# Kernel tuning notes

Hardware: AMD Instinct MI355X
Metric: run time of the kernel (lower is better)

## Reference

```python
import jax, jax.numpy as jnp
import numpy as np

EPS_BN = 1e-5
EPS_NORM = 1e-12


def _conv1x1(x, W, b):
    # x: (B,C,H,W), W: (O,C), b: (O,)
    return jnp.einsum('bchw,oc->bohw', x, W) + b[None, :, None, None]


def _bn_train(x, gamma, beta):
    # BatchNorm2d in training mode: biased batch statistics over (N,H,W)
    m = x.mean(axis=(0, 2, 3), keepdims=True)
    v = x.var(axis=(0, 2, 3), keepdims=True)
    return (x - m) / jnp.sqrt(v + EPS_BN) * gamma[None, :, None, None] + beta[None, :, None, None]


def _l2norm(x):
    # F.normalize(dim=-1)
    return x / jnp.maximum(jnp.linalg.norm(x, axis=-1, keepdims=True), EPS_NORM)


def setup_inputs() -> dict:
    key = jax.random.key(0)
    ks = jax.random.split(key, 12)
    B, C, H, Wd = 8, 256, 64, 64
    HD, M = 128, 10
    s = 0.02
    inp = {
        'key': jax.random.normal(ks[0], (B, C, H, Wd), jnp.float32),
        'query': jax.random.normal(ks[1], (B, C, H, Wd), jnp.float32),
        'W_theta': jax.random.normal(ks[2], (HD, C), jnp.float32) * s,
        'b_theta': jnp.zeros((HD,), jnp.float32),
        'W_phi': jax.random.normal(ks[3], (HD, C), jnp.float32) * s,
        'b_phi': jnp.zeros((HD,), jnp.float32),
        'W_g': jax.random.normal(ks[4], (HD, C), jnp.float32) * s,
        'b_g': jnp.zeros((HD,), jnp.float32),
        'W_pc': jax.random.normal(ks[5], (HD, C), jnp.float32) * s,
        'b_pc': jnp.zeros((HD,), jnp.float32),
        'gamma_pc': jnp.ones((HD,), jnp.float32),
        'beta_pc': jnp.zeros((HD,), jnp.float32),
        'W_heads': jax.random.normal(ks[6], (M, HD), jnp.float32) * s,
        'W_o': jax.random.normal(ks[7], (C, HD), jnp.float32) * s,
        'b_o': jnp.zeros((C,), jnp.float32),
        'gamma_o': jnp.ones((C,), jnp.float32),
        'beta_o': jnp.zeros((C,), jnp.float32),
    }
    return inp


def reference(key, query, W_theta, b_theta, W_phi, b_phi, W_g, b_g,
              W_pc, b_pc, gamma_pc, beta_pc, W_heads, W_o, b_o, gamma_o, beta_o):
    B, C, H, Wd = key.shape
    HD = W_theta.shape[0]
    HW = H * Wd

    # --- non-local self-attention branch ---
    theta = _conv1x1(key, W_theta, b_theta).reshape(B, HD, HW)
    phi = _conv1x1(key, W_phi, b_phi).reshape(B, HD, HW)
    g = _conv1x1(key, W_g, b_g).reshape(B, HD, HW)
    att = jax.nn.softmax(jnp.einsum('bdn,bdm->bnm', theta, phi), axis=-1)  # (B,HW,HW)
    nlsa_out = jnp.einsum('bnm,bdm->bdn', att, g).reshape(B, HD, H, Wd)

    # --- prototype features ---
    key_f = jax.nn.relu(_bn_train(_conv1x1(key, W_pc, b_pc), gamma_pc, beta_pc))
    key_f = key_f.transpose(0, 2, 3, 1).reshape(B, HW, HD)  # (B,n,d); query_ == key_f

    mhw = jax.nn.softmax(key_f @ W_heads.T, axis=1)          # softmax over spatial dim
    protos = jnp.einsum('bnm,bnd->bmd', mhw, key_f)          # (B,M,d)

    # --- losses (training path) ---
    pn = _l2norm(protos)
    M = pn.shape[1]
    dis = 1.0 - ((pn[:, None, :, :] - pn[:, :, None, :]) ** 2)[None]  # (1,B,M,M,d)
    dis = dis * (dis > 0).astype(dis.dtype)
    dis = jnp.triu(dis, k=1)  # triu over last two dims (M,d), as torch.triu does
    dis_loss = (dis.sum(axis=1).sum(axis=1) * 2.0 / (M * (M - 1))).mean()
    cst_loss = ((pn[1:] - pn[:-1]) ** 2).sum(-1).mean()

    score = jnp.einsum('bnd,bmd->bnm', key_f, pn)            # (B,n,M)
    sp = jax.nn.softmax(score, axis=-1)                      # softmax over protos
    new_q = _l2norm(jnp.einsum('bnm,bmd->bnd', sp, pn))      # (B,n,d)

    idx = jnp.argmax(sp, axis=-1)                            # top-1 proto per position
    pos = pn[jnp.arange(B)[:, None], idx]                    # (B,n,d)
    fea_loss = jnp.mean((key_f - pos) ** 2)

    # --- output projection ---
    uq = new_q.transpose(0, 2, 1).reshape(B, HD, H, Wd) + nlsa_out
    out = jax.nn.relu(_bn_train(_conv1x1(uq, W_o, b_o), gamma_o, beta_o)) + query
    return out, fea_loss, cst_loss, dis_loss
```

## Files before the change

kernel.cpp:

```cpp
#include <hip/hip_runtime.h>
#include <stdint.h>

#define BB 8
#define CC 256
#define HDIM 128
#define NHW 4096
#define MM 10
#define OUTN (BB*CC*NHW)

typedef uint32_t u32;
typedef unsigned short u16;
using f32x4 = __attribute__((ext_vector_type(4))) float;
using bfv8  = __attribute__((ext_vector_type(8))) short;

__device__ __forceinline__ u16 f2bf(float f){
  union { float f; u32 u; } v; v.f = f;
  u32 u = v.u;
  u32 r = (u + 0x7fffu + ((u >> 16) & 1u)) >> 16;
  return (u16)r;
}

__device__ __forceinline__ float bf2f(u16 h){
  union { u32 u; float f; } v; v.u = ((u32)h) << 16; return v.f;
}

__device__ __forceinline__ f32x4 mfma16(bfv8 a, bfv8 b, f32x4 c){
  return __builtin_amdgcn_mfma_f32_16x16x32_bf16(a, b, c, 0, 0, 0);
}

__device__ __forceinline__ void gload16(const void* g, void* l){
  __builtin_amdgcn_global_load_lds((const __attribute__((address_space(1))) unsigned int*)g,
                                   (__attribute__((address_space(3))) unsigned int*)l, 16, 0, 0);
}

__global__ __launch_bounds__(256) void k0_keyt(const float* __restrict__ key, u16* __restrict__ keyT){
  __shared__ u16 sm[64][73];
  int blk = blockIdx.x;
  int b = blk & 7; int r = blk >> 3; int ct = r & 3; int nt = r >> 2;
  int n0 = nt*64, c0 = ct*64;
  int t = threadIdx.x; int nl = t & 63; int cl0 = t >> 6;
#pragma unroll
  for (int i = 0; i < 16; ++i){
    int cl = i*4 + cl0;
    sm[cl][nl] = f2bf(key[(size_t)(b*CC + c0 + cl)*NHW + n0 + nl]);
  }
  __syncthreads();
#pragma unroll
  for (int i = 0; i < 2; ++i){
    int j = i*256 + t; int nl2 = j >> 3; int c8 = j & 7;
    __align__(16) u16 tmp[8];
#pragma unroll
    for (int k = 0; k < 8; ++k) tmp[k] = sm[c8*8 + k][nl2];
    *(uint4*)&keyT[(size_t)(b*NHW + n0 + nl2)*CC + c0 + c8*8] = *(uint4*)tmp;
  }
}

__global__ __launch_bounds__(256) void k0b_w(const float* __restrict__ Wth, const float* __restrict__ Wph,
                                             const float* __restrict__ Wg, const float* __restrict__ Wpc,
                                             const float* __restrict__ Wo,
                                             u16* __restrict__ Wbf, u16* __restrict__ Wobf,
                                             float* __restrict__ stats, float* __restrict__ protos){
  int flat = blockIdx.x*256 + threadIdx.x;
  if (flat < 1540) stats[flat] = 0.f;
  if (flat < BB*MM*HDIM) protos[flat] = 0.f;
  int base = flat*4;
  u16 o4[4]; uint2 pk;
  if (base < 512*256){
    int o = base >> 8, c = base & 255;
    const float* srcs[4] = {Wth, Wph, Wg, Wpc};
    const float* sp = srcs[o >> 7] + (size_t)(o & 127)*256 + c;
#pragma unroll
    for (int j=0;j<4;++j) o4[j] = f2bf(sp[j]);
    pk.x = (u32)o4[0] | ((u32)o4[1]<<16); pk.y = (u32)o4[2] | ((u32)o4[3]<<16);
    *(uint2*)&Wbf[base] = pk;
  } else {
    int b2 = base - 512*256;
    const float* sp = Wo + b2;
#pragma unroll
    for (int j=0;j<4;++j) o4[j] = f2bf(sp[j]);
    pk.x = (u32)o4[0] | ((u32)o4[1]<<16); pk.y = (u32)o4[2] | ((u32)o4[3]<<16);
    *(uint2*)&Wobf[b2] = pk;
  }
}

__global__ __launch_bounds__(256) void k1_conv4(const u16* __restrict__ keyT, const u16* __restrict__ Wbf,
    const float* __restrict__ bth, const float* __restrict__ bph, const float* __restrict__ bg, const float* __restrict__ bpc,
    u16* __restrict__ thetaT, u16* __restrict__ phiT, u16* __restrict__ gN, float* __restrict__ pcraw)
{
  __shared__ __align__(16) u16 lds[64*256];
  int blk = blockIdx.x;
  int b = blk & 7; int nt = blk >> 3; int n0 = nt*64;
  int t = threadIdx.x; int w = t >> 6; int l = t & 63;
  int l15 = l & 15, l4 = l >> 4;
  const u16* src = keyT + (size_t)(b*NHW + n0)*CC;
#pragma unroll
  for (int i = 0; i < 8; ++i){
    int c = w*8 + i;
    int row = c*2 + (l >> 5);
    int wl = (l & 31) ^ (row & 7);
    gload16(src + (size_t)row*256 + wl*8, &lds[c*512]);
  }
  __syncthreads();
  int wn = w & 1, wo = w >> 1;
  bfv8 a[2][8];
#pragma unroll
  for (int nb = 0; nb < 2; ++nb)
#pragma unroll
    for (int kb = 0; kb < 8; ++kb){
      int row = wn*32 + nb*16 + l15;
      int wd = (kb*4 + l4) ^ (row & 7);
      a[nb][kb] = *(const bfv8*)&lds[row*256 + wd*8];
    }
  const float* bias[4] = {bth, bph, bg, bpc};
  const u16* wpbase = Wbf + (size_t)(wo*16*16 + l15)*256 + l4*8;
  bfv8 wc[8], wnx[8];
#pragma unroll
  for (int kb = 0; kb < 8; ++kb) wc[kb] = *(const bfv8*)&wpbase[kb*32];
  for (int ob = 0; ob < 16; ++ob){
    if (ob < 15){
      const u16* wp = wpbase + (size_t)(ob+1)*16*256;
#pragma unroll
      for (int kb = 0; kb < 8; ++kb) wnx[kb] = *(const bfv8*)&wp[kb*32];
    }
    f32x4 acc[2] = {{0,0,0,0},{0,0,0,0}};
#pragma unroll
    for (int kb = 0; kb < 8; ++kb){
      acc[0] = mfma16(a[0][kb], wc[kb], acc[0]);
      acc[1] = mfma16(a[1][kb], wc[kb], acc[1]);
    }
    int obg = wo*16 + ob;
    int seg = obg >> 3;
    int oo = (obg & 7)*16 + l15;
    float bv = bias[seg][oo];
#pragma unroll
    for (int nb = 0; nb < 2; ++nb)
#pragma unroll
      for (int rr = 0; rr < 4; ++rr){
        int n = n0 + wn*32 + nb*16 + l4*4 + rr;
        float v = acc[nb][rr] + bv;
        size_t off = ((size_t)(b*NHW + n))*HDIM + oo;
        if      (seg == 0) thetaT[off] = f2bf(v);
        else if (seg == 1) phiT[off]   = f2bf(v);
        else if (seg == 2) gN[off]     = f2bf(v);
        else               pcraw[off]  = v;
      }
#pragma unroll
    for (int kb = 0; kb < 8; ++kb) wc[kb] = wnx[kb];
  }
}

__global__ __launch_bounds__(256) void k1b_gt(const u16* __restrict__ gN, u16* __restrict__ gT){
  __shared__ __align__(16) u16 lds[64][72];
  int blk = blockIdx.x;
  int b = blk & 7; int r = blk >> 3; int nt = r & 63; int dt = r >> 6;
  int n0 = nt*64, d0 = dt*64;
  int t = threadIdx.x;
#pragma unroll
  for (int i = 0; i < 2; ++i){
    int seg = i*256 + t; int row = seg >> 3; int sg = seg & 7;
    *(uint4*)&lds[row][sg*8] = *(const uint4*)&gN[(size_t)(b*NHW + n0 + row)*HDIM + d0 + sg*8];
  }
  __syncthreads();
  int dr = t >> 2, ns = (t & 3)*16;
  __align__(16) u16 tmp[16];
#pragma unroll
  for (int j = 0; j < 16; ++j) tmp[j] = lds[ns + j][dr];
  u16* dst = gT + (size_t)(b*HDIM + d0 + dr)*NHW + n0 + ns;
  *(uint4*)&dst[0] = *(uint4*)&tmp[0];
  *(uint4*)&dst[8] = *(uint4*)&tmp[8];
}

__global__ __launch_bounds__(256) void k2_pcstats(const float* __restrict__ pcraw, float* __restrict__ stats){
  int blk = blockIdx.x;
  int b = blk >> 5; int ch = blk & 31; int n0 = ch*128;
  int t = threadIdx.x; int d = t & 127; int j = t >> 7;
  float s = 0, ss = 0;
  const float* p = pcraw + (size_t)(b*NHW + n0)*HDIM;
  for (int i = 0; i < 64; ++i){ float v = p[(size_t)(i*2 + j)*HDIM + d]; s += v; ss += v*v; }
  __shared__ float red[2][256];
  red[0][t] = s; red[1][t] = ss;
  __syncthreads();
  if (t < 128){
    atomicAdd(&stats[d],       red[0][t] + red[0][t+128]);
    atomicAdd(&stats[128 + d], red[1][t] + red[1][t+128]);
  }
}

__global__ __launch_bounds__(256) void k2b_keyf(const float* __restrict__ pcraw, const float* __restrict__ stats,
                                                const float* __restrict__ gamma, const float* __restrict__ beta,
                                                float* __restrict__ keyf){
  int idx = blockIdx.x*256 + threadIdx.x;
  int base = idx*4; int d0 = base & 127;
  f32x4 v = *(const f32x4*)&pcraw[base];
  f32x4 o;
#pragma unroll
  for (int j = 0; j < 4; ++j){
    int d = d0 + j;
    float mean = stats[d] * (1.f/32768.f);
    float var  = stats[128+d] * (1.f/32768.f) - mean*mean;
    if (var < 0.f) var = 0.f;
    float rstd = rsqrtf(var + 1e-5f);
    float x = (v[j] - mean) * rstd * gamma[d] + beta[d];
    o[j] = x > 0.f ? x : 0.f;
  }
  *(f32x4*)&keyf[base] = o;
}

__global__ __launch_bounds__(256) void k3_attn(const u16* __restrict__ thetaT, const u16* __restrict__ phiT,
                                               const u16* __restrict__ gT,
                                               u16* __restrict__ nl0, u16* __restrict__ nl1,
                                               u16* __restrict__ nl2, u16* __restrict__ nl3,
                                               float* __restrict__ lsumP){
  __shared__ __align__(16) u16 K2[2][32*128];
  __shared__ __align__(16) u16 V2[2][128*32];
  __shared__ __align__(16) u16 P[4][32*40];
  int blk = blockIdx.x;
  int b = blk & 7; int r1 = blk >> 3; int qt = r1 & 31; int split = r1 >> 5;
  int n0 = qt*128;
  int t = threadIdx.x; int w = t >> 6; int l = t & 63;
  int l15 = l & 15, l4 = l >> 4;
  bfv8 q[2][4];
#pragma unroll
  for (int nb = 0; nb < 2; ++nb){
    const u16* qp = thetaT + (size_t)(b*NHW + n0 + w*32 + nb*16 + l15)*HDIM + l4*8;
#pragma unroll
    for (int kb = 0; kb < 4; ++kb) q[nb][kb] = *(const bfv8*)&qp[kb*32];
  }
  float lsum[2][4];
  f32x4 acco[2][8];
#pragma unroll
  for (int nb=0; nb<2; ++nb){
#pragma unroll
    for (int rr=0; rr<4; ++rr) lsum[nb][rr] = 0.f;
#pragma unroll
    for (int db=0; db<8; ++db) acco[nb][db] = {0,0,0,0};
  }
  const u16* Kg = phiT + (size_t)b*NHW*HDIM;
  const u16* Vg = gT   + (size_t)b*HDIM*NHW;
  int mt0 = split*32;

#define STAGE(bf, mt) {                                                        \
    int m0 = (mt)*32;                                                          \
  _Pragma("unroll")                                                            \
    for (int i = 0; i < 2; ++i){                                               \
      int c = w*2 + i;                                                         \
      int row = c*4 + (l >> 4);                                                \
      int wl = (l & 15) ^ (row & 7);                                           \
      gload16(Kg + (size_t)(m0 + row)*HDIM + wl*8, &K2[bf][c*512]);            \
    }                                                                          \
  _Pragma("unroll")                                                            \
    for (int i = 0; i < 2; ++i){                                               \
      int c = w*2 + i;                                                         \
      int row = c*16 + (l >> 2);                                               \
      int wl = (l & 3) ^ (row & 3);                                            \
      gload16(Vg + (size_t)row*NHW + m0 + wl*8, &V2[bf][c*512]);               \
    }                                                                          \
  }

  STAGE(0, mt0);
  __syncthreads();
  int cur = 0;
  for (int it = 0; it < 32; ++it){
    if (it < 31) STAGE(cur^1, mt0 + it + 1);
    f32x4 s[2][2];
#pragma unroll
    for (int nb=0;nb<2;++nb){ s[nb][0] = {0,0,0,0}; s[nb][1] = {0,0,0,0}; }
    __builtin_amdgcn_s_setprio(1);
#pragma unroll
    for (int kb = 0; kb < 4; ++kb){
#pragma unroll
      for (int mb = 0; mb < 2; ++mb){
        int krow = mb*16 + l15;
        int kw = (kb*4 + l4) ^ (krow & 7);
        bfv8 kf = *(const bfv8*)&K2[cur][krow*128 + kw*8];
        s[0][mb] = mfma16(q[0][kb], kf, s[0][mb]);
        s[1][mb] = mfma16(q[1][kb], kf, s[1][mb]);
      }
    }
    __builtin_amdgcn_s_setprio(0);
#pragma unroll
    for (int nb = 0; nb < 2; ++nb)
#pragma unroll
      for (int mb = 0; mb < 2; ++mb)
#pragma unroll
        for (int rr = 0; rr < 4; ++rr){
          float p = __expf(s[nb][mb][rr]);
          lsum[nb][rr] += p;
          int prow = nb*16 + l4*4 + rr;
          int pcol = mb*16 + l15;
          P[w][prow*40 + pcol] = f2bf(p);
        }
    bfv8 pa[2];
#pragma unroll
    for (int nb=0;nb<2;++nb)
      pa[nb] = *(const bfv8*)&P[w][(nb*16 + l15)*40 + l4*8];
    __builtin_amdgcn_s_setprio(1);
#pragma unroll
    for (int db = 0; db < 8; ++db){
      int vrow = db*16 + l15;
      int vw = l4 ^ (vrow & 3);
      bfv8 vf = *(const bfv8*)&V2[cur][vrow*32 + vw*8];
      acco[0][db] = mfma16(pa[0], vf, acco[0][db]);
      acco[1][db] = mfma16(pa[1], vf, acco[1][db]);
    }
    __builtin_amdgcn_s_setprio(0);
    __syncthreads();
    cur ^= 1;
  }
#undef STAGE
  u16* nlsaP = (split==0) ? nl0 : (split==1) ? nl1 : (split==2) ? nl2 : nl3;
#pragma unroll
  for (int nb = 0; nb < 2; ++nb)
#pragma unroll
    for (int rr = 0; rr < 4; ++rr){
      float v = lsum[nb][rr];
      v += __shfl_xor(v, 1); v += __shfl_xor(v, 2); v += __shfl_xor(v, 4); v += __shfl_xor(v, 8);
      int n = n0 + w*32 + nb*16 + l4*4 + rr;
      if (l15 == 0) lsumP[(size_t)(split*8 + b)*NHW + n] = v;
      u16* op = nlsaP + ((size_t)(b*NHW + n))*HDIM;
#pragma unroll
      for (int db = 0; db < 8; ++db)
        op[db*16 + l15] = f2bf(acco[nb][db][rr]);
    }
}

__global__ __launch_bounds__(256) void k4_protos(const float* __restrict__ keyf, const float* __restrict__ Wh,
                                                 float* __restrict__ protos){
  __shared__ float wh[10][128];
  __shared__ float e[128][12];
  __shared__ float pacc[10][128];
  int blk = blockIdx.x; int b = blk & 7; int ns = blk >> 3;
  int n0 = ns*128;
  int t = threadIdx.x;
  for (int i = t; i < 1280; i += 256) wh[i>>7][i&127] = Wh[i];
  __syncthreads();
  const float* kf = keyf + ((size_t)b*NHW + n0)*HDIM;
  {
    int nn = t >> 1; int mh = (t & 1)*5;
    const f32x4* row = (const f32x4*)&kf[(size_t)nn*HDIM];
    float s5[5];
#pragma unroll
    for (int m = 0; m < 5; ++m) s5[m] = 0.f;
    for (int d4 = 0; d4 < 32; ++d4){
      f32x4 kv = row[d4];
#pragma unroll
      for (int m = 0; m < 5; ++m){
        f32x4 wv = *(const f32x4*)&wh[mh+m][d4*4];
        s5[m] += kv[0]*wv[0] + kv[1]*wv[1] + kv[2]*wv[2] + kv[3]*wv[3];
      }
    }
#pragma unroll
    for (int m = 0; m < 5; ++m) e[nn][mh+m] = __expf(s5[m]);
  }
  __syncthreads();
  int d = t & 127, j = t >> 7;
  float acc[10];
#pragma unroll
  for (int m = 0; m < 10; ++m) acc[m] = 0.f;
  for (int i = 0; i < 64; ++i){
    int n = j*64 + i;
    float kv = kf[(size_t)n*HDIM + d];
#pragma unroll
    for (int m = 0; m < 10; ++m) acc[m] += e[n][m]*kv;
  }
  if (j == 1){
#pragma unroll
    for (int m = 0; m < 10; ++m) pacc[m][d] = acc[m];
  }
  __syncthreads();
  if (j == 0){
#pragma unroll
    for (int m = 0; m < 10; ++m)
      atomicAdd(&protos[(size_t)(b*MM + m)*HDIM + d], acc[m] + pacc[m][d]);
  }
}

__global__ __launch_bounds__(64) void k5a_norm(float* __restrict__ protos){
  int row = blockIdx.x;
  int t = threadIdx.x;
  float v0 = protos[row*128 + t];
  float v1 = protos[row*128 + 64 + t];
  float ss = v0*v0 + v1*v1;
#pragma unroll
  for (int msk = 1; msk < 64; msk <<= 1) ss += __shfl_xor(ss, msk);
  float inv = 1.f / fmaxf(sqrtf(ss), 1e-12f);
  protos[row*128 + t]      = v0*inv;
  protos[row*128 + 64 + t] = v1*inv;
}

__global__ __launch_bounds__(128) void k5b_loss(const float* __restrict__ pn, float* __restrict__ stats){
  __shared__ float p0[10][128];
  __shared__ float p1[10][128];
  __shared__ float rd[2][2];
  int b = blockIdx.x;
  int t = threadIdx.x;
  for (int i = t; i < 1280; i += 128) p0[i>>7][i&127] = pn[(size_t)b*1280 + i];
  if (b < 7)
    for (int i = t; i < 1280; i += 128) p1[i>>7][i&127] = pn[(size_t)(b+1)*1280 + i];
  __syncthreads();
  int d = t;
  float dacc = 0.f;
#pragma unroll
  for (int m1 = 0; m1 < 10; ++m1){
    float a = p0[m1][d];
#pragma unroll
    for (int m2 = 0; m2 < 10; ++m2){
      if (d >= m2 + 1){
        float df = a - p0[m2][d];
        float v = 1.f - df*df;
        if (v > 0.f) dacc += v;
      }
    }
  }
  float cacc = 0.f;
  if (b < 7){
#pragma unroll
    for (int m = 0; m < 10; ++m){
      float df = p1[m][d] - p0[m][d];
      cacc += df*df;
    }
  }
#pragma unroll
  for (int msk = 1; msk < 64; msk <<= 1){ dacc += __shfl_xor(dacc, msk); cacc += __shfl_xor(cacc, msk); }
  int wv = t >> 6, ln = t & 63;
  if (ln == 0){ rd[0][wv] = dacc; rd[1][wv] = cacc; }
  __syncthreads();
  if (t == 0){
    atomicAdd(&stats[1537], rd[0][0] + rd[0][1]);
    atomicAdd(&stats[1538], rd[1][0] + rd[1][1]);
  }
}

__global__ __launch_bounds__(64) void k6_newq(const float* __restrict__ keyf, const float* __restrict__ pn,
                                              const u16* __restrict__ nl0, const u16* __restrict__ nl1,
                                              const u16* __restrict__ nl2, const u16* __restrict__ nl3,
                                              const float* __restrict__ lsumP,
                                              u16* __restrict__ uqbf, float* __restrict__ fea_acc){
  __shared__ float pnl[10][128];
  int blk = blockIdx.x;
  int b = blk & 7; int nt = blk >> 3;
  int t = threadIdx.x;
  for (int i = t; i < 1280; i += 64) pnl[i>>7][i&127] = pn[(size_t)b*1280 + i];
  __syncthreads();
  int n = nt*64 + t;
  const float* kf = keyf + (size_t)(b*NHW + n)*HDIM;
  float s[10];
#pragma unroll
  for (int m = 0; m < 10; ++m) s[m] = 0;
  for (int d4 = 0; d4 < 32; ++d4){
    f32x4 kv = *(const f32x4*)&kf[d4*4];
#pragma unroll
    for (int m = 0; m < 10; ++m){
      f32x4 pv = *(const f32x4*)&pnl[m][d4*4];
      s[m] += kv[0]*pv[0]+kv[1]*pv[1]+kv[2]*pv[2]+kv[3]*pv[3];
    }
  }
  float mx = s[0]; int idx = 0;
#pragma unroll
  for (int m = 1; m < 10; ++m) if (s[m] > mx){ mx = s[m]; idx = m; }
  float S_ = 0, sp[10];
#pragma unroll
  for (int m = 0; m < 10; ++m){ float ev = __expf(s[m]-mx); sp[m] = ev; S_ += ev; }
  float invS = 1.f/S_;
#pragma unroll
  for (int m = 0; m < 10; ++m) sp[m] *= invS;
  float ssq = 0, fea = 0;
  for (int d4 = 0; d4 < 32; ++d4){
    f32x4 kv = *(const f32x4*)&kf[d4*4];
    f32x4 a = {0,0,0,0};
#pragma unroll
    for (int m = 0; m < 10; ++m){
      f32x4 pv = *(const f32x4*)&pnl[m][d4*4];
      a[0] += sp[m]*pv[0]; a[1] += sp[m]*pv[1]; a[2] += sp[m]*pv[2]; a[3] += sp[m]*pv[3];
    }
    ssq += a[0]*a[0]+a[1]*a[1]+a[2]*a[2]+a[3]*a[3];
    f32x4 pb = *(const f32x4*)&pnl[idx][d4*4];
    float e0 = kv[0]-pb[0], e1 = kv[1]-pb[1], e2 = kv[2]-pb[2], e3 = kv[3]-pb[3];
    fea += e0*e0+e1*e1+e2*e2+e3*e3;
  }
  float inv = 1.f / fmaxf(sqrtf(ssq), 1e-12f);
  float ls = lsumP[(size_t)b*NHW + n] + lsumP[(size_t)(8+b)*NHW + n]
           + lsumP[(size_t)(16+b)*NHW + n] + lsumP[(size_t)(24+b)*NHW + n];
  float invl = 1.f/ls;
  const u16* na0 = nl0 + (size_t)(b*NHW + n)*HDIM;
  const u16* na1 = nl1 + (size_t)(b*NHW + n)*HDIM;
  const u16* na2 = nl2 + (size_t)(b*NHW + n)*HDIM;
  const u16* na3 = nl3 + (size_t)(b*NHW + n)*HDIM;
  u16* uo = uqbf + (size_t)(b*NHW + n)*HDIM;
  for (int d4 = 0; d4 < 32; ++d4){
    f32x4 a = {0,0,0,0};
#pragma unroll
    for (int m = 0; m < 10; ++m){
      f32x4 pv = *(const f32x4*)&pnl[m][d4*4];
      a[0] += sp[m]*pv[0]; a[1] += sp[m]*pv[1]; a[2] += sp[m]*pv[2]; a[3] += sp[m]*pv[3];
    }
    uint2 r0 = *(const uint2*)&na0[d4*4];
    uint2 r1 = *(const uint2*)&na1[d4*4];
    uint2 r2 = *(const uint2*)&na2[d4*4];
    uint2 r3 = *(const uint2*)&na3[d4*4];
    u16 o4[4];
#pragma unroll
    for (int j = 0; j < 4; ++j){
      u32 word0 = (j < 2) ? r0.x : r0.y;  u32 word1 = (j < 2) ? r1.x : r1.y;
      u32 word2 = (j < 2) ? r2.x : r2.y;  u32 word3 = (j < 2) ? r3.x : r3.y;
      int sh = (j & 1)*16;
      float nv = bf2f((u16)(word0 >> sh)) + bf2f((u16)(word1 >> sh))
               + bf2f((u16)(word2 >> sh)) + bf2f((u16)(word3 >> sh));
      o4[j] = f2bf(a[j]*inv + nv*invl);
    }
    uint2 pk; pk.x = (u32)o4[0] | ((u32)o4[1]<<16); pk.y = (u32)o4[2] | ((u32)o4[3]<<16);
    *(uint2*)&uo[d4*4] = pk;
  }
#pragma unroll
  for (int msk = 1; msk < 64; msk <<= 1) fea += __shfl_xor(fea, msk);
  if (t == 0) atomicAdd(fea_acc, fea);
}

__global__ __launch_bounds__(256) void k7_convo(const u16* __restrict__ uqbf, const u16* __restrict__ Wobf,
                                                const float* __restrict__ bo, float* __restrict__ convo){
  __shared__ __align__(16) u16 lds[64*128];
  int blk = blockIdx.x;
  int b = blk & 7; int nt = blk >> 3; int n0 = nt*64;
  int t = threadIdx.x; int w = t >> 6; int l = t & 63; int l15 = l&15, l4 = l>>4;
  const u16* src = uqbf + (size_t)(b*NHW + n0)*HDIM;
#pragma unroll
  for (int i = 0; i < 4; ++i){
    int c = w*4 + i;
    int row = c*4 + (l >> 4);
    int wl = (l & 15) ^ (row & 7);
    gload16(src + (size_t)row*128 + wl*8, &lds[c*512]);
  }
  __syncthreads();
  int wn = w & 1, wo = w >> 1;
  bfv8 a[2][4];
#pragma unroll
  for (int nb = 0; nb < 2; ++nb)
#pragma unroll
    for (int kb = 0; kb < 4; ++kb){
      int row = wn*32 + nb*16 + l15;
      int wd = (kb*4 + l4) ^ (row & 7);
      a[nb][kb] = *(const bfv8*)&lds[row*128 + wd*8];
    }
  const u16* wpbase = Wobf + (size_t)(wo*8*16 + l15)*128 + l4*8;
  bfv8 wc[4], wnx[4];
#pragma unroll
  for (int kb = 0; kb < 4; ++kb) wc[kb] = *(const bfv8*)&wpbase[kb*32];
  for (int ob = 0; ob < 8; ++ob){
    if (ob < 7){
      const u16* wp = wpbase + (size_t)(ob+1)*16*128;
#pragma unroll
      for (int kb = 0; kb < 4; ++kb) wnx[kb] = *(const bfv8*)&wp[kb*32];
    }
    f32x4 acc[2] = {{0,0,0,0},{0,0,0,0}};
#pragma unroll
    for (int kb = 0; kb < 4; ++kb){
      acc[0] = mfma16(a[0][kb], wc[kb], acc[0]);
      acc[1] = mfma16(a[1][kb], wc[kb], acc[1]);
    }
    int obg = wo*8 + ob;
    int oc = obg*16 + l15;
    float bv = bo[oc];
#pragma unroll
    for (int nb = 0; nb < 2; ++nb)
#pragma unroll
      for (int rr = 0; rr < 4; ++rr){
        int n = n0 + wn*32 + nb*16 + l4*4 + rr;
        convo[(size_t)(b*NHW + n)*CC + oc] = acc[nb][rr] + bv;
      }
#pragma unroll
    for (int kb = 0; kb < 4; ++kb) wc[kb] = wnx[kb];
  }
}

__global__ __launch_bounds__(256) void k8_ostats(const float* __restrict__ convo, float* __restrict__ stats){
  int blk = blockIdx.x;
  int b = blk >> 5; int ch = blk & 31; int n0 = ch*128;
  int t = threadIdx.x;
  float s = 0, ss = 0;
  const float* p = convo + (size_t)(b*NHW + n0)*CC;
  for (int i = 0; i < 128; ++i){ float v = p[(size_t)i*CC + t]; s += v; ss += v*v; }
  atomicAdd(&stats[512 + t], s);
  atomicAdd(&stats[768 + t], ss);
}

__global__ void k8a_fin(float* stats, float* dout){
  int c = threadIdx.x;
  float mean = stats[512+c] * (1.f/32768.f);
  float var  = stats[768+c] * (1.f/32768.f) - mean*mean;
  if (var < 0.f) var = 0.f;
  stats[1024+c] = mean;
  stats[1280+c] = rsqrtf(var + 1e-5f);
  if (c == 0){
    dout[OUTN]   = stats[1536] * (1.f/4194304.f);
    dout[OUTN+1] = stats[1538] * (1.f/70.f);
    dout[OUTN+2] = stats[1537] * (2.f/90.f) * (1.f/1280.f);
  }
}

__global__ __launch_bounds__(256) void k9_out(const float* __restrict__ convo, const float* __restrict__ stats,
                                              const float* __restrict__ gamma, const float* __restrict__ beta,
                                              const float* __restrict__ query, float* __restrict__ dout){
  __shared__ __align__(16) float lds[32*260];
  int blk = blockIdx.x; int b = blk & 7; int nt = blk >> 3; int n0 = nt*32;
  int t = threadIdx.x;
  const float* src = convo + (size_t)(b*NHW + n0)*CC;
#pragma unroll
  for (int i = 0; i < 8; ++i){
    int seg = i*256 + t; int row = seg >> 6; int sg = seg & 63;
    *(f32x4*)&lds[row*260 + sg*4] = *(const f32x4*)&src[(size_t)row*CC + sg*4];
  }
  __syncthreads();
  int nn = t & 31, og = t >> 5;
  for (int i = 0; i < 32; ++i){
    int oc = og*32 + i;
    float v = lds[nn*260 + oc];
    v = (v - stats[1024+oc]) * stats[1280+oc] * gamma[oc] + beta[oc];
    v = fmaxf(v, 0.f);
    size_t off = (size_t)(b*CC + oc)*NHW + n0 + nn;
    dout[off] = v + query[off];
  }
}

extern "C" void kernel_launch(void* const* d_in, const int* in_sizes, int n_in,
                              void* d_out, int out_size, void* d_ws, size_t ws_size,
                              hipStream_t stream) {
  const float* key   = (const float*)d_in[0];
  const float* query = (const float*)d_in[1];
  const float* Wth = (const float*)d_in[2];
  const float* bth = (const float*)d_in[3];
  const float* Wph = (const float*)d_in[4];
  const float* bph = (const float*)d_in[5];
  const float* Wg  = (const float*)d_in[6];
  const float* bg  = (const float*)d_in[7];
  const float* Wpc = (const float*)d_in[8];
  const float* bpc = (const float*)d_in[9];
  const float* gpc = (const float*)d_in[10];
  const float* bepc= (const float*)d_in[11];
  const float* Wh  = (const float*)d_in[12];
  const float* Wo  = (const float*)d_in[13];
  const float* bo  = (const float*)d_in[14];
  const float* go  = (const float*)d_in[15];
  const float* beo = (const float*)d_in[16];

  char* ws = (char*)d_ws;
  u16*   keyT   = (u16*)  (ws + 0);
  u16*   nlsa0  = (u16*)  (ws + 0);
  u16*   nlsa1  = (u16*)  (ws + 8388608);
  u16*   thetaT = (u16*)  (ws + 16777216);
  u16*   phiT   = (u16*)  (ws + 25165824);
  u16*   gN     = (u16*)  (ws + 33554432);
  float* lsum   = (float*)(ws + 33554432);
  u16*   gT     = (u16*)  (ws + 41943040);
  float* pcraw  = (float*)(ws + 50331648);
  u16*   nlsa2  = (u16*)  (ws + 50331648);
  u16*   nlsa3  = (u16*)  (ws + 58720256);
  float* keyf   = (float*)(ws + 67108864);
  u16*   uqbf   = (u16*)  (ws + 83886080);
  float* convo  = (float*)(ws + 92274688);
  u16*   Wbf    = (u16*)  (ws + 125829120);
  u16*   Wobf   = (u16*)  (ws + 126091264);
  float* protos = (float*)(ws + 126156800);
  float* stats  = (float*)(ws + 126197760);
  float* dout   = (float*)d_out;

  k0_keyt<<<2048,256,0,stream>>>(key, keyT);
  k0b_w<<<160,256,0,stream>>>(Wth, Wph, Wg, Wpc, Wo, Wbf, Wobf, stats, protos);
  k1_conv4<<<512,256,0,stream>>>(keyT, Wbf, bth, bph, bg, bpc, thetaT, phiT, gN, pcraw);
  k1b_gt<<<1024,256,0,stream>>>(gN, gT);
  k2_pcstats<<<256,256,0,stream>>>(pcraw, stats);
  k2b_keyf<<<4096,256,0,stream>>>(pcraw, stats, gpc, bepc, keyf);
  k3_attn<<<1024,256,0,stream>>>(thetaT, phiT, gT, nlsa0, nlsa1, nlsa2, nlsa3, lsum);
  k4_protos<<<256,256,0,stream>>>(keyf, Wh, protos);
  k5a_norm<<<80,64,0,stream>>>(protos);
  k5b_loss<<<8,128,0,stream>>>(protos, stats);
  k6_newq<<<512,64,0,stream>>>(keyf, protos, nlsa0, nlsa1, nlsa2, nlsa3, lsum, uqbf, &stats[1536]);
  k7_convo<<<512,256,0,stream>>>(uqbf, Wobf, bo, convo);
  k8_ostats<<<256,256,0,stream>>>(convo, stats);
  k8a_fin<<<1,256,0,stream>>>(stats, dout);
  k9_out<<<1024,256,0,stream>>>(convo, stats, go, beo, query, dout);
}
```

Baseline: 427.0 us.

## Retile attention to 64 queries per wave, keep P in registers, shrink conv output to bf16

The attention kernel now gives each wave 64 query rows instead of 32 and computes S transposed, so the exponentiated scores can feed the PV MFMA straight from registers through the 16x16x16 bf16 instruction, with no round trip through LDS. The exp is replaced by exp2, with log2(e) folded into theta when it is written. It also merges the prototype normalisation and loss kernels, widens k6 and keeps keyf in registers across its passes. The output-conv intermediate is stored as bf16 instead of fp32 to halve its traffic. The risks are higher register pressure in the attention kernel and reduced precision in the stored conv output and its BN statistics.

```diff
diff --git a/kernel.cpp b/kernel.cpp
--- a/kernel.cpp
+++ b/kernel.cpp
@@ -12,6 +12,13 @@
 typedef unsigned short u16;
 using f32x4 = __attribute__((ext_vector_type(4))) float;
 using bfv8  = __attribute__((ext_vector_type(8))) short;
+using bfv4  = __attribute__((ext_vector_type(4))) short;
+
+#if __has_builtin(__builtin_amdgcn_mfma_f32_16x16x16bf16_1k)
+#define HAS16 1
+#else
+#define HAS16 0
+#endif
 
 __device__ __forceinline__ u16 f2bf(float f){
   union { float f; u32 u; } v; v.f = f;
@@ -26,6 +33,18 @@
 
 __device__ __forceinline__ f32x4 mfma16(bfv8 a, bfv8 b, f32x4 c){
   return __builtin_amdgcn_mfma_f32_16x16x32_bf16(a, b, c, 0, 0, 0);
+}
+
+__device__ __forceinline__ u32 cvtpk(float a, float b){
+  u32 r; asm("v_cvt_pk_bf16_f32 %0, %1, %2" : "=v"(r) : "v"(a), "v"(b)); return r;
+}
+
+__device__ __forceinline__ float fexp2(float x){
+#if __has_builtin(__builtin_amdgcn_exp2f)
+  return __builtin_amdgcn_exp2f(x);
+#else
+  return exp2f(x);
+#endif
 }
 
 __device__ __forceinline__ void gload16(const void* g, void* l){
@@ -139,7 +158,7 @@
         int n = n0 + wn*32 + nb*16 + l4*4 + rr;
         float v = acc[nb][rr] + bv;
         size_t off = ((size_t)(b*NHW + n))*HDIM + oo;
-        if      (seg == 0) thetaT[off] = f2bf(v);
+        if      (seg == 0) thetaT[off] = f2bf(v * 1.44269504f);
         else if (seg == 1) phiT[off]   = f2bf(v);
         else if (seg == 2) gN[off]     = f2bf(v);
         else               pcraw[off]  = v;
@@ -206,34 +225,35 @@
   *(f32x4*)&keyf[base] = o;
 }
 
-__global__ __launch_bounds__(256) void k3_attn(const u16* __restrict__ thetaT, const u16* __restrict__ phiT,
+__global__ __launch_bounds__(256, 2) void k3_attn(const u16* __restrict__ thetaT, const u16* __restrict__ phiT,
                                                const u16* __restrict__ gT,
                                                u16* __restrict__ nl0, u16* __restrict__ nl1,
                                                u16* __restrict__ nl2, u16* __restrict__ nl3,
                                                float* __restrict__ lsumP){
   __shared__ __align__(16) u16 K2[2][32*128];
   __shared__ __align__(16) u16 V2[2][128*32];
-  __shared__ __align__(16) u16 P[4][32*40];
+#if !HAS16
+  __shared__ __align__(16) u16 P[4][64*40];
+#endif
   int blk = blockIdx.x;
-  int b = blk & 7; int r1 = blk >> 3; int qt = r1 & 31; int split = r1 >> 5;
-  int n0 = qt*128;
+  int b = blk & 7; int qt = (blk >> 3) & 15; int split = blk >> 7;
+  int n0 = qt*256;
   int t = threadIdx.x; int w = t >> 6; int l = t & 63;
   int l15 = l & 15, l4 = l >> 4;
-  bfv8 q[2][4];
-#pragma unroll
-  for (int nb = 0; nb < 2; ++nb){
-    const u16* qp = thetaT + (size_t)(b*NHW + n0 + w*32 + nb*16 + l15)*HDIM + l4*8;
-#pragma unroll
-    for (int kb = 0; kb < 4; ++kb) q[nb][kb] = *(const bfv8*)&qp[kb*32];
-  }
-  float lsum[2][4];
-  f32x4 acco[2][8];
-#pragma unroll
-  for (int nb=0; nb<2; ++nb){
-#pragma unroll
-    for (int rr=0; rr<4; ++rr) lsum[nb][rr] = 0.f;
-#pragma unroll
-    for (int db=0; db<8; ++db) acco[nb][db] = {0,0,0,0};
+  bfv8 qf[4][4];
+#pragma unroll
+  for (int qb = 0; qb < 4; ++qb){
+    const u16* qp = thetaT + (size_t)(b*NHW + n0 + w*64 + qb*16 + l15)*HDIM + l4*8;
+#pragma unroll
+    for (int kb = 0; kb < 4; ++kb) qf[qb][kb] = *(const bfv8*)&qp[kb*32];
+  }
+  float lsum[4];
+  f32x4 acco[4][8];
+#pragma unroll
+  for (int qb = 0; qb < 4; ++qb){
+    lsum[qb] = 0.f;
+#pragma unroll
+    for (int db = 0; db < 8; ++db) acco[qb][db] = {0,0,0,0};
   }
   const u16* Kg = phiT + (size_t)b*NHW*HDIM;
   const u16* Vg = gT   + (size_t)b*HDIM*NHW;
@@ -262,9 +282,11 @@
   int cur = 0;
   for (int it = 0; it < 32; ++it){
     if (it < 31) STAGE(cur^1, mt0 + it + 1);
-    f32x4 s[2][2];
-#pragma unroll
-    for (int nb=0;nb<2;++nb){ s[nb][0] = {0,0,0,0}; s[nb][1] = {0,0,0,0}; }
+    f32x4 s[2][4];
+#pragma unroll
+    for (int mb = 0; mb < 2; ++mb)
+#pragma unroll
+      for (int qb = 0; qb < 4; ++qb) s[mb][qb] = {0,0,0,0};
     __builtin_amdgcn_s_setprio(1);
 #pragma unroll
     for (int kb = 0; kb < 4; ++kb){
@@ -273,55 +295,91 @@
         int krow = mb*16 + l15;
         int kw = (kb*4 + l4) ^ (krow & 7);
         bfv8 kf = *(const bfv8*)&K2[cur][krow*128 + kw*8];
-        s[0][mb] = mfma16(q[0][kb], kf, s[0][mb]);
-        s[1][mb] = mfma16(q[1][kb], kf, s[1][mb]);
+#pragma unroll
+        for (int qb = 0; qb < 4; ++qb)
+          s[mb][qb] = mfma16(kf, qf[qb][kb], s[mb][qb]);
       }
     }
     __builtin_amdgcn_s_setprio(0);
-#pragma unroll
-    for (int nb = 0; nb < 2; ++nb)
-#pragma unroll
-      for (int mb = 0; mb < 2; ++mb)
-#pragma unroll
-        for (int rr = 0; rr < 4; ++rr){
-          float p = __expf(s[nb][mb][rr]);
-          lsum[nb][rr] += p;
-          int prow = nb*16 + l4*4 + rr;
-          int pcol = mb*16 + l15;
-          P[w][prow*40 + pcol] = f2bf(p);
-        }
-    bfv8 pa[2];
-#pragma unroll
-    for (int nb=0;nb<2;++nb)
-      pa[nb] = *(const bfv8*)&P[w][(nb*16 + l15)*40 + l4*8];
+#if HAS16
+    bfv4 pa[2][4];
+#pragma unroll
+    for (int mb = 0; mb < 2; ++mb)
+#pragma unroll
+      for (int qb = 0; qb < 4; ++qb){
+        float p0 = fexp2(s[mb][qb][0]);
+        float p1 = fexp2(s[mb][qb][1]);
+        float p2 = fexp2(s[mb][qb][2]);
+        float p3 = fexp2(s[mb][qb][3]);
+        lsum[qb] += (p0+p1)+(p2+p3);
+        union { uint2 u; bfv4 v; } cv;
+        cv.u.x = cvtpk(p0, p1); cv.u.y = cvtpk(p2, p3);
+        pa[mb][qb] = cv.v;
+      }
+    __builtin_amdgcn_s_setprio(1);
+#pragma unroll
+    for (int db = 0; db < 8; ++db){
+      int vrow = db*16 + l15;
+#pragma unroll
+      for (int mb = 0; mb < 2; ++mb){
+        int sg = mb*2 + (l4 >> 1);
+        int ph = ((sg ^ (vrow & 3))*8 + (l4 & 1)*4);
+        bfv4 vf = *(const bfv4*)&V2[cur][vrow*32 + ph];
+#pragma unroll
+        for (int qb = 0; qb < 4; ++qb)
+          acco[qb][db] = __builtin_amdgcn_mfma_f32_16x16x16bf16_1k(pa[mb][qb], vf, acco[qb][db], 0, 0, 0);
+      }
+    }
+    __builtin_amdgcn_s_setprio(0);
+#else
+    u16* Pw = &P[w][0];
+#pragma unroll
+    for (int mb = 0; mb < 2; ++mb)
+#pragma unroll
+      for (int qb = 0; qb < 4; ++qb){
+        float p0 = fexp2(s[mb][qb][0]);
+        float p1 = fexp2(s[mb][qb][1]);
+        float p2 = fexp2(s[mb][qb][2]);
+        float p3 = fexp2(s[mb][qb][3]);
+        lsum[qb] += (p0+p1)+(p2+p3);
+        uint2 pk; pk.x = cvtpk(p0, p1); pk.y = cvtpk(p2, p3);
+        *(uint2*)&Pw[(qb*16 + l15)*40 + mb*16 + l4*4] = pk;
+      }
+    bfv8 pa[4];
+#pragma unroll
+    for (int qb = 0; qb < 4; ++qb)
+      pa[qb] = *(const bfv8*)&Pw[(qb*16 + l15)*40 + l4*8];
     __builtin_amdgcn_s_setprio(1);
 #pragma unroll
     for (int db = 0; db < 8; ++db){
       int vrow = db*16 + l15;
       int vw = l4 ^ (vrow & 3);
       bfv8 vf = *(const bfv8*)&V2[cur][vrow*32 + vw*8];
-      acco[0][db] = mfma16(pa[0], vf, acco[0][db]);
-      acco[1][db] = mfma16(pa[1], vf, acco[1][db]);
+#pragma unroll
+      for (int qb = 0; qb < 4; ++qb)
+        acco[qb][db] = mfma16(pa[qb], vf, acco[qb][db]);
     }
     __builtin_amdgcn_s_setprio(0);
+#endif
     __syncthreads();
     cur ^= 1;
   }
 #undef STAGE
   u16* nlsaP = (split==0) ? nl0 : (split==1) ? nl1 : (split==2) ? nl2 : nl3;
 #pragma unroll
-  for (int nb = 0; nb < 2; ++nb)
+  for (int qb = 0; qb < 4; ++qb){
+    float v = lsum[qb];
+    v += __shfl_xor(v, 16); v += __shfl_xor(v, 32);
+    if (l < 16) lsumP[(size_t)(split*8 + b)*NHW + n0 + w*64 + qb*16 + l] = v;
 #pragma unroll
     for (int rr = 0; rr < 4; ++rr){
-      float v = lsum[nb][rr];
-      v += __shfl_xor(v, 1); v += __shfl_xor(v, 2); v += __shfl_xor(v, 4); v += __shfl_xor(v, 8);
-      int n = n0 + w*32 + nb*16 + l4*4 + rr;
-      if (l15 == 0) lsumP[(size_t)(split*8 + b)*NHW + n] = v;
+      int n = n0 + w*64 + qb*16 + l4*4 + rr;
       u16* op = nlsaP + ((size_t)(b*NHW + n))*HDIM;
 #pragma unroll
       for (int db = 0; db < 8; ++db)
-        op[db*16 + l15] = f2bf(acco[nb][db][rr]);
-    }
+        op[db*16 + l15] = f2bf(acco[qb][db][rr]);
+    }
+  }
 }
 
 __global__ __launch_bounds__(256) void k4_protos(const float* __restrict__ keyf, const float* __restrict__ Wh,
@@ -375,38 +433,35 @@
   }
 }
 
-__global__ __launch_bounds__(64) void k5a_norm(float* __restrict__ protos){
-  int row = blockIdx.x;
-  int t = threadIdx.x;
-  float v0 = protos[row*128 + t];
-  float v1 = protos[row*128 + 64 + t];
-  float ss = v0*v0 + v1*v1;
-#pragma unroll
-  for (int msk = 1; msk < 64; msk <<= 1) ss += __shfl_xor(ss, msk);
-  float inv = 1.f / fmaxf(sqrtf(ss), 1e-12f);
-  protos[row*128 + t]      = v0*inv;
-  protos[row*128 + 64 + t] = v1*inv;
-}
-
-__global__ __launch_bounds__(128) void k5b_loss(const float* __restrict__ pn, float* __restrict__ stats){
-  __shared__ float p0[10][128];
-  __shared__ float p1[10][128];
+__global__ __launch_bounds__(128) void k5_pnloss(const float* __restrict__ protos, float* __restrict__ pnorm,
+                                                 float* __restrict__ stats){
+  __shared__ float pr[20][128];
   __shared__ float rd[2][2];
   int b = blockIdx.x;
-  int t = threadIdx.x;
-  for (int i = t; i < 1280; i += 128) p0[i>>7][i&127] = pn[(size_t)b*1280 + i];
-  if (b < 7)
-    for (int i = t; i < 1280; i += 128) p1[i>>7][i&127] = pn[(size_t)(b+1)*1280 + i];
+  int t = threadIdx.x; int wv = t >> 6; int ln = t & 63;
+  int nrows = (b < 7) ? 20 : 10;
+  for (int r = wv; r < nrows; r += 2){
+    int g = (r < 10) ? (b*10 + r) : ((b+1)*10 + (r-10));
+    float v0 = protos[g*128 + ln];
+    float v1 = protos[g*128 + 64 + ln];
+    float ss = v0*v0 + v1*v1;
+#pragma unroll
+    for (int msk = 1; msk < 64; msk <<= 1) ss += __shfl_xor(ss, msk);
+    float inv = 1.f / fmaxf(sqrtf(ss), 1e-12f);
+    v0 *= inv; v1 *= inv;
+    pr[r][ln] = v0; pr[r][64+ln] = v1;
+    if (r < 10){ pnorm[g*128 + ln] = v0; pnorm[g*128 + 64 + ln] = v1; }
+  }
   __syncthreads();
   int d = t;
   float dacc = 0.f;
 #pragma unroll
   for (int m1 = 0; m1 < 10; ++m1){
-    float a = p0[m1][d];
+    float a = pr[m1][d];
 #pragma unroll
     for (int m2 = 0; m2 < 10; ++m2){
       if (d >= m2 + 1){
-        float df = a - p0[m2][d];
+        float df = a - pr[m2][d];
         float v = 1.f - df*df;
         if (v > 0.f) dacc += v;
       }
@@ -416,13 +471,12 @@
   if (b < 7){
 #pragma unroll
     for (int m = 0; m < 10; ++m){
-      float df = p1[m][d] - p0[m][d];
+      float df = pr[10+m][d] - pr[m][d];
       cacc += df*df;
     }
   }
 #pragma unroll
   for (int msk = 1; msk < 64; msk <<= 1){ dacc += __shfl_xor(dacc, msk); cacc += __shfl_xor(cacc, msk); }
-  int wv = t >> 6, ln = t & 63;
   if (ln == 0){ rd[0][wv] = dacc; rd[1][wv] = cacc; }
   __syncthreads();
   if (t == 0){
@@ -431,28 +485,33 @@
   }
 }
 
-__global__ __launch_bounds__(64) void k6_newq(const float* __restrict__ keyf, const float* __restrict__ pn,
+__global__ __launch_bounds__(128, 2) void k6_newq(const float* __restrict__ keyf, const float* __restrict__ pn,
                                               const u16* __restrict__ nl0, const u16* __restrict__ nl1,
                                               const u16* __restrict__ nl2, const u16* __restrict__ nl3,
                                               const float* __restrict__ lsumP,
                                               u16* __restrict__ uqbf, float* __restrict__ fea_acc){
-  __shared__ float pnl[10][128];
+  __shared__ float pnl[10][132];
+  __shared__ float red[2];
   int blk = blockIdx.x;
   int b = blk & 7; int nt = blk >> 3;
   int t = threadIdx.x;
-  for (int i = t; i < 1280; i += 64) pnl[i>>7][i&127] = pn[(size_t)b*1280 + i];
-  __syncthreads();
-  int n = nt*64 + t;
+  for (int i = t; i < 1280; i += 128) pnl[i>>7][i&127] = pn[(size_t)b*1280 + i];
+  __syncthreads();
+  int n = nt*128 + t;
   const float* kf = keyf + (size_t)(b*NHW + n)*HDIM;
+  f32x4 kv[32];
+#pragma unroll
+  for (int d4 = 0; d4 < 32; ++d4) kv[d4] = *(const f32x4*)&kf[d4*4];
   float s[10];
 #pragma unroll
-  for (int m = 0; m < 10; ++m) s[m] = 0;
+  for (int m = 0; m < 10; ++m) s[m] = 0.f;
+#pragma unroll
   for (int d4 = 0; d4 < 32; ++d4){
-    f32x4 kv = *(const f32x4*)&kf[d4*4];
+    f32x4 k = kv[d4];
 #pragma unroll
     for (int m = 0; m < 10; ++m){
       f32x4 pv = *(const f32x4*)&pnl[m][d4*4];
-      s[m] += kv[0]*pv[0]+kv[1]*pv[1]+kv[2]*pv[2]+kv[3]*pv[3];
+      s[m] += k[0]*pv[0]+k[1]*pv[1]+k[2]*pv[2]+k[3]*pv[3];
     }
   }
   float mx = s[0]; int idx = 0;
@@ -465,8 +524,9 @@
 #pragma unroll
   for (int m = 0; m < 10; ++m) sp[m] *= invS;
   float ssq = 0, fea = 0;
+#pragma unroll
   for (int d4 = 0; d4 < 32; ++d4){
-    f32x4 kv = *(const f32x4*)&kf[d4*4];
+    f32x4 k = kv[d4];
     f32x4 a = {0,0,0,0};
 #pragma unroll
     for (int m = 0; m < 10; ++m){
@@ -475,8 +535,9 @@
     }
     ssq += a[0]*a[0]+a[1]*a[1]+a[2]*a[2]+a[3]*a[3];
     f32x4 pb = *(const f32x4*)&pnl[idx][d4*4];
-    float e0 = kv[0]-pb[0], e1 = kv[1]-pb[1], e2 = kv[2]-pb[2], e3 = kv[3]-pb[3];
+    float e0 = k[0]-pb[0], e1 = k[1]-pb[1], e2 = k[2]-pb[2], e3 = k[3]-pb[3];
     fea += e0*e0+e1*e1+e2*e2+e3*e3;
+    kv[d4] = a;
   }
   float inv = 1.f / fmaxf(sqrtf(ssq), 1e-12f);
   float ls = lsumP[(size_t)b*NHW + n] + lsumP[(size_t)(8+b)*NHW + n]
@@ -487,13 +548,8 @@
   const u16* na2 = nl2 + (size_t)(b*NHW + n)*HDIM;
   const u16* na3 = nl3 + (size_t)(b*NHW + n)*HDIM;
   u16* uo = uqbf + (size_t)(b*NHW + n)*HDIM;
+#pragma unroll
   for (int d4 = 0; d4 < 32; ++d4){
-    f32x4 a = {0,0,0,0};
-#pragma unroll
-    for (int m = 0; m < 10; ++m){
-      f32x4 pv = *(const f32x4*)&pnl[m][d4*4];
-      a[0] += sp[m]*pv[0]; a[1] += sp[m]*pv[1]; a[2] += sp[m]*pv[2]; a[3] += sp[m]*pv[3];
-    }
     uint2 r0 = *(const uint2*)&na0[d4*4];
     uint2 r1 = *(const uint2*)&na1[d4*4];
     uint2 r2 = *(const uint2*)&na2[d4*4];
@@ -506,18 +562,21 @@
       int sh = (j & 1)*16;
       float nv = bf2f((u16)(word0 >> sh)) + bf2f((u16)(word1 >> sh))
                + bf2f((u16)(word2 >> sh)) + bf2f((u16)(word3 >> sh));
-      o4[j] = f2bf(a[j]*inv + nv*invl);
+      o4[j] = f2bf(kv[d4][j]*inv + nv*invl);
     }
     uint2 pk; pk.x = (u32)o4[0] | ((u32)o4[1]<<16); pk.y = (u32)o4[2] | ((u32)o4[3]<<16);
     *(uint2*)&uo[d4*4] = pk;
   }
 #pragma unroll
   for (int msk = 1; msk < 64; msk <<= 1) fea += __shfl_xor(fea, msk);
-  if (t == 0) atomicAdd(fea_acc, fea);
+  int wv = t >> 6;
+  if ((t & 63) == 0) red[wv] = fea;
+  __syncthreads();
+  if (t == 0) atomicAdd(fea_acc, red[0] + red[1]);
 }
 
 __global__ __launch_bounds__(256) void k7_convo(const u16* __restrict__ uqbf, const u16* __restrict__ Wobf,
-                                                const float* __restrict__ bo, float* __restrict__ convo){
+                                                const float* __restrict__ bo, u16* __restrict__ convo){
   __shared__ __align__(16) u16 lds[64*128];
   int blk = blockIdx.x;
   int b = blk & 7; int nt = blk >> 3; int n0 = nt*64;
@@ -565,20 +624,20 @@
 #pragma unroll
       for (int rr = 0; rr < 4; ++rr){
         int n = n0 + wn*32 + nb*16 + l4*4 + rr;
-        convo[(size_t)(b*NHW + n)*CC + oc] = acc[nb][rr] + bv;
+        convo[(size_t)(b*NHW + n)*CC + oc] = f2bf(acc[nb][rr] + bv);
       }
 #pragma unroll
     for (int kb = 0; kb < 4; ++kb) wc[kb] = wnx[kb];
   }
 }
 
-__global__ __launch_bounds__(256) void k8_ostats(const float* __restrict__ convo, float* __restrict__ stats){
+__global__ __launch_bounds__(256) void k8_ostats(const u16* __restrict__ convo, float* __restrict__ stats){
   int blk = blockIdx.x;
   int b = blk >> 5; int ch = blk & 31; int n0 = ch*128;
   int t = threadIdx.x;
   float s = 0, ss = 0;
-  const float* p = convo + (size_t)(b*NHW + n0)*CC;
-  for (int i = 0; i < 128; ++i){ float v = p[(size_t)i*CC + t]; s += v; ss += v*v; }
+  const u16* p = convo + (size_t)(b*NHW + n0)*CC;
+  for (int i = 0; i < 128; ++i){ float v = bf2f(p[(size_t)i*CC + t]); s += v; ss += v*v; }
   atomicAdd(&stats[512 + t], s);
   atomicAdd(&stats[768 + t], ss);
 }
@@ -597,17 +656,24 @@
   }
 }
 
-__global__ __launch_bounds__(256) void k9_out(const float* __restrict__ convo, const float* __restrict__ stats,
+__global__ __launch_bounds__(256) void k9_out(const u16* __restrict__ convo, const float* __restrict__ stats,
                                               const float* __restrict__ gamma, const float* __restrict__ beta,
                                               const float* __restrict__ query, float* __restrict__ dout){
   __shared__ __align__(16) float lds[32*260];
   int blk = blockIdx.x; int b = blk & 7; int nt = blk >> 3; int n0 = nt*32;
   int t = threadIdx.x;
-  const float* src = convo + (size_t)(b*NHW + n0)*CC;
-#pragma unroll
-  for (int i = 0; i < 8; ++i){
-    int seg = i*256 + t; int row = seg >> 6; int sg = seg & 63;
-    *(f32x4*)&lds[row*260 + sg*4] = *(const f32x4*)&src[(size_t)row*CC + sg*4];
+  const u16* src = convo + (size_t)(b*NHW + n0)*CC;
+#pragma unroll
+  for (int i = 0; i < 4; ++i){
+    int seg = i*256 + t; int row = seg >> 5; int sg = seg & 31;
+    uint4 pk = *(const uint4*)&src[(size_t)row*CC + sg*8];
+    float* dst = &lds[row*260 + sg*8];
+    u32 ws[4] = {pk.x, pk.y, pk.z, pk.w};
+#pragma unroll
+    for (int j = 0; j < 4; ++j){
+      dst[j*2]   = bf2f((u16)(ws[j] & 0xffffu));
+      dst[j*2+1] = bf2f((u16)(ws[j] >> 16));
+    }
   }
   __syncthreads();
   int nn = t & 31, og = t >> 5;
@@ -656,11 +722,12 @@
   u16*   nlsa3  = (u16*)  (ws + 58720256);
   float* keyf   = (float*)(ws + 67108864);
   u16*   uqbf   = (u16*)  (ws + 83886080);
-  float* convo  = (float*)(ws + 92274688);
-  u16*   Wbf    = (u16*)  (ws + 125829120);
-  u16*   Wobf   = (u16*)  (ws + 126091264);
-  float* protos = (float*)(ws + 126156800);
-  float* stats  = (float*)(ws + 126197760);
+  u16*   convo  = (u16*)  (ws + 92274688);
+  u16*   Wbf    = (u16*)  (ws + 109051904);
+  u16*   Wobf   = (u16*)  (ws + 109314048);
+  float* protos = (float*)(ws + 109379584);
+  float* pnorm  = (float*)(ws + 109420544);
+  float* stats  = (float*)(ws + 109461504);
   float* dout   = (float*)d_out;
 
   k0_keyt<<<2048,256,0,stream>>>(key, keyT);
@@ -669,11 +736,10 @@
   k1b_gt<<<1024,256,0,stream>>>(gN, gT);
   k2_pcstats<<<256,256,0,stream>>>(pcraw, stats);
   k2b_keyf<<<4096,256,0,stream>>>(pcraw, stats, gpc, bepc, keyf);
-  k3_attn<<<1024,256,0,stream>>>(thetaT, phiT, gT, nlsa0, nlsa1, nlsa2, nlsa3, lsum);
+  k3_attn<<<512,256,0,stream>>>(thetaT, phiT, gT, nlsa0, nlsa1, nlsa2, nlsa3, lsum);
   k4_protos<<<256,256,0,stream>>>(keyf, Wh, protos);
-  k5a_norm<<<80,64,0,stream>>>(protos);
-  k5b_loss<<<8,128,0,stream>>>(protos, stats);
-  k6_newq<<<512,64,0,stream>>>(keyf, protos, nlsa0, nlsa1, nlsa2, nlsa3, lsum, uqbf, &stats[1536]);
+  k5_pnloss<<<8,128,0,stream>>>(protos, pnorm, stats);
+  k6_newq<<<256,128,0,stream>>>(keyf, pnorm, nlsa0, nlsa1, nlsa2, nlsa3, lsum, uqbf, &stats[1536]);
   k7_convo<<<512,256,0,stream>>>(uqbf, Wobf, bo, convo);
   k8_ostats<<<256,256,0,stream>>>(convo, stats);
   k8a_fin<<<1,256,0,stream>>>(stats, dout);
```

After: 560.8 us. +31.3%, slower.
